# Kernel optimization log

Measured on AMD Instinct MI355X. Metric: run time of the kernel, lower is better.

## Reference

```python
import jax, jax.numpy as jnp
import numpy as np

LN_EPS = 1e-5

def _conv2d(x, w, b, pad):
    # x: [B,C,H,W], w: [O,I,kh,kw] -> [B,O,H,W]
    y = jax.lax.conv_general_dilated(
        x, w, window_strides=(1, 1), padding=[(pad, pad), (pad, pad)],
        dimension_numbers=('NCHW', 'OIHW', 'NCHW'))
    return y + b[None, :, None, None]

def setup_inputs() -> dict:
    key = jax.random.key(0)
    ks = jax.random.split(key, 12)
    B, C, H, W = 4, 256, 64, 64
    D = 64  # inner_projection
    s_in = 1.0 / np.sqrt(C)
    s_d1 = 1.0 / np.sqrt(D)
    s_d3 = 1.0 / np.sqrt(D * 9)
    return {
        'x':     jax.random.normal(ks[0], (B, C, H, W), jnp.float32),
        'w_in':  jax.random.normal(ks[1], (D, C, 1, 1), jnp.float32) * s_in,
        'b_in':  jnp.zeros((D,), jnp.float32),
        'wq':    jax.random.normal(ks[2], (D, D, 3, 3), jnp.float32) * s_d3,
        'bq':    jnp.zeros((D,), jnp.float32),
        'wk':    jax.random.normal(ks[3], (D, D, 3, 3), jnp.float32) * s_d3,
        'bk':    jnp.zeros((D,), jnp.float32),
        'wv':    jax.random.normal(ks[4], (D, D, 3, 3), jnp.float32) * s_d3,
        'bv':    jnp.zeros((D,), jnp.float32),
        'w_out': jax.random.normal(ks[5], (C, D, 1, 1), jnp.float32) * s_d1,
        'b_out': jnp.zeros((C,), jnp.float32),
        'gamma': jax.random.normal(ks[6], (1,), jnp.float32) * 0.1,
        'ln_w':  jnp.ones((C,), jnp.float32),
        'ln_b':  jnp.zeros((C,), jnp.float32),
    }

def _attention(q, k, v):
    # full-pixel attention, NO 1/sqrt(d) scale (matches source)
    B, C, H, W = v.shape
    N = H * W
    qf = q.reshape(B, -1, N)   # [B,d,N]
    kf = k.reshape(B, -1, N)
    vf = v.reshape(B, -1, N)
    energy = jnp.einsum('bci,bcj->bij', qf, kf)      # [B,N,N] = Q^T K
    attn = jax.nn.softmax(energy, axis=-1)
    out = jnp.einsum('bcj,bij->bci', vf, attn)        # V @ attn^T
    return out.reshape(B, C, H, W)

def _layernorm2d(x, w, b):
    # normalize over channel dim per pixel (LayerNorm2d)
    mu = jnp.mean(x, axis=1, keepdims=True)
    var = jnp.var(x, axis=1, keepdims=True)
    xn = (x - mu) * jax.lax.rsqrt(var + LN_EPS)
    return xn * w[None, :, None, None] + b[None, :, None, None]

def reference(x, w_in, b_in, wq, bq, wk, bk, wv, bv, w_out, b_out, gamma, ln_w, ln_b):
    att = _conv2d(x, w_in, b_in, 0)          # inner projection [B,D,H,W]
    q = _conv2d(att, wq, bq, 1)
    k = _conv2d(att, wk, bk, 1)
    v = _conv2d(att, wv, bv, 1)
    att = _attention(q, k, v)
    att = _conv2d(att, w_out, b_out, 0)       # outer projection [B,C,H,W]
    return _layernorm2d(gamma * x + att, ln_w, ln_b)
```

## Files before the change

kernel.cpp:

```cpp
#include <hip/hip_runtime.h>
#include <hip/hip_bf16.h>

#define BB 4
#define CC 256
#define DD 64
#define HH 64
#define WW 64
#define NN 4096
#define NSPLIT 4

typedef __hip_bfloat16 bf16;
typedef __attribute__((ext_vector_type(8))) short bf16x8;
typedef __attribute__((ext_vector_type(4))) float f32x4;
typedef __attribute__((ext_vector_type(4))) short s16x4;

#define MFMA16(a, b, c) __builtin_amdgcn_mfma_f32_16x16x32_bf16(a, b, c, 0, 0, 0)

static __device__ __forceinline__ float ldin(const void* p, size_t i, bool isb) {
  return isb ? __bfloat162float(((const bf16*)p)[i]) : ((const float*)p)[i];
}
static __device__ __forceinline__ void stout(void* p, size_t i, float v, bool isb) {
  if (isb) ((bf16*)p)[i] = __float2bfloat16(v);
  else     ((float*)p)[i] = v;
}
static __device__ __forceinline__ unsigned pack2(bf16 a, bf16 b) {
  unsigned short ua = *reinterpret_cast<unsigned short*>(&a);
  unsigned short ub = *reinterpret_cast<unsigned short*>(&b);
  return (unsigned)ua | ((unsigned)ub << 16);
}

__global__ void k_flag(const unsigned* __restrict__ lnw, int* __restrict__ flag) {
  if (threadIdx.x == 0) flag[0] = (lnw[0] == 0x3F803F80u) ? 1 : 0;
}

__global__ __launch_bounds__(256) void k_wt(
    const void* __restrict__ wq, const void* __restrict__ wk,
    const void* __restrict__ wv, const void* __restrict__ w_in,
    const void* __restrict__ w_out,
    bf16* __restrict__ Wth, bf16* __restrict__ Wtl,
    bf16* __restrict__ Win_h, bf16* __restrict__ Win_l,
    bf16* __restrict__ Wo_h, bf16* __restrict__ Wo_l,
    const int* __restrict__ flag) {
  const bool isb = flag[0] != 0;
  int u = blockIdx.x * 256 + threadIdx.x;
  if (u < 110592) {
    int c3 = u / 36864, rem = u % 36864;
    int tap = rem / 4096, r2 = rem % 4096;
    int oc = r2 >> 6, ic = r2 & 63;
    const void* w = (c3 == 0) ? wq : ((c3 == 1) ? wk : wv);
    float v = ldin(w, (size_t)oc * 576 + ic * 9 + tap, isb);
    bf16 h = __float2bfloat16(v);
    Wth[u] = h;
    Wtl[u] = __float2bfloat16(v - __bfloat162float(h));
  } else if (u < 126976) {
    int v2 = u - 110592;
    float v = ldin(w_in, v2, isb);
    bf16 h = __float2bfloat16(v);
    Win_h[v2] = h;
    Win_l[v2] = __float2bfloat16(v - __bfloat162float(h));
  } else {
    int v2 = u - 126976;
    float v = ldin(w_out, v2, isb);
    bf16 h = __float2bfloat16(v);
    Wo_h[v2] = h;
    Wo_l[v2] = __float2bfloat16(v - __bfloat162float(h));
  }
}

__global__ __launch_bounds__(256) void k_conv_in(
    const void* __restrict__ x,
    const bf16* __restrict__ Win_h, const bf16* __restrict__ Win_l,
    const void* __restrict__ bias, bf16* __restrict__ att_h,
    bf16* __restrict__ att_l, const int* __restrict__ flag) {
  __shared__ __align__(16) short Xh[64 * 64];
  __shared__ __align__(16) short Xl[64 * 64];
  const bool isb = flag[0] != 0;
  const int b = blockIdx.y, n0 = blockIdx.x * 64;
  const int t = threadIdx.x;
  const int w = t >> 6, lane = t & 63, quad = lane >> 4, l16 = lane & 15;
  const int l7 = l16 & 7;
  const size_t xoff = (size_t)b * CC * NN;
  f32x4 acc[4];
  #pragma unroll
  for (int nt = 0; nt < 4; ++nt)
    #pragma unroll
    for (int r = 0; r < 4; ++r)
      acc[nt][r] = ldin(bias, w * 16 + quad * 4 + r, isb);
  for (int c0 = 0; c0 < CC; c0 += 64) {
    __syncthreads();
    #pragma unroll
    for (int i = 0; i < 8; ++i) {
      int u = t + i * 256;
      int dd = u >> 6, n = u & 63;
      float v0 = ldin(x, xoff + (size_t)(c0 + 2 * dd) * NN + n0 + n, isb);
      float v1 = ldin(x, xoff + (size_t)(c0 + 2 * dd + 1) * NN + n0 + n, isb);
      bf16 h0 = __float2bfloat16(v0), h1 = __float2bfloat16(v1);
      bf16 l0 = __float2bfloat16(v0 - __bfloat162float(h0));
      bf16 l1 = __float2bfloat16(v1 - __bfloat162float(h1));
      int cs = ((dd >> 2) ^ (n & 7)) * 8 + ((2 * dd) & 7);
      *(unsigned*)&Xh[n * 64 + cs] = pack2(h0, h1);
      *(unsigned*)&Xl[n * 64 + cs] = pack2(l0, l1);
    }
    __syncthreads();
    #pragma unroll
    for (int kc = 0; kc < 2; ++kc) {
      size_t woff = (size_t)(w * 16 + l16) * 256 + c0 + kc * 32 + quad * 8;
      bf16x8 wh = *(const bf16x8*)(Win_h + woff);
      bf16x8 wl = *(const bf16x8*)(Win_l + woff);
      const int xo = ((kc * 4 + quad) ^ l7) * 8;
      #pragma unroll
      for (int nt = 0; nt < 4; ++nt) {
        int rn = nt * 16 + l16;
        bf16x8 xh = *(const bf16x8*)&Xh[rn * 64 + xo];
        bf16x8 xl = *(const bf16x8*)&Xl[rn * 64 + xo];
        acc[nt] = MFMA16(wh, xh, acc[nt]);
        acc[nt] = MFMA16(wh, xl, acc[nt]);
        acc[nt] = MFMA16(wl, xh, acc[nt]);
      }
    }
  }
  #pragma unroll
  for (int nt = 0; nt < 4; ++nt) {
    size_t off = ((size_t)b * NN + n0 + nt * 16 + l16) * DD + w * 16 + quad * 4;
    bf16 h[4], l[4];
    #pragma unroll
    for (int r = 0; r < 4; ++r) {
      float v = acc[nt][r];
      h[r] = __float2bfloat16(v);
      l[r] = __float2bfloat16(v - __bfloat162float(h[r]));
    }
    uint2 hv = make_uint2(pack2(h[0], h[1]), pack2(h[2], h[3]));
    uint2 lv = make_uint2(pack2(l[0], l[1]), pack2(l[2], l[3]));
    *(uint2*)&att_h[off] = hv;
    *(uint2*)&att_l[off] = lv;
  }
}

__global__ __launch_bounds__(256) void k_conv3(
    const bf16* __restrict__ att_h, const bf16* __restrict__ att_l,
    const bf16* __restrict__ Wth, const bf16* __restrict__ Wtl,
    const void* __restrict__ bq, const void* __restrict__ bk,
    const void* __restrict__ bv,
    bf16* __restrict__ qth, bf16* __restrict__ qtl,
    bf16* __restrict__ kth, bf16* __restrict__ ktl,
    bf16* __restrict__ vt, const int* __restrict__ flag) {
  __shared__ __align__(16) short Ah[3 * 66 * 72];
  __shared__ __align__(16) short Al[3 * 66 * 72];
  __shared__ float o_s[64 * 65];
  const bool isb = flag[0] != 0;
  const int y = blockIdx.x, b = blockIdx.y, c3 = blockIdx.z;
  const int t = threadIdx.x;
  const int w = t >> 6, lane = t & 63, quad = lane >> 4, l16 = lane & 15;
  const uint4 z4 = make_uint4(0, 0, 0, 0);
  #pragma unroll
  for (int r = 0; r < 3; ++r) {
    int yp = y + r - 1;
    bool ok = (unsigned)yp < 64u;
    const uint4* sh = (const uint4*)(att_h + ((size_t)b * NN + (size_t)yp * 64) * DD);
    const uint4* sl = (const uint4*)(att_l + ((size_t)b * NN + (size_t)yp * 64) * DD);
    #pragma unroll
    for (int ii = 0; ii < 2; ++ii) {
      int u = t + ii * 256;
      int xx = u >> 3, icg = (u & 7) * 8;
      uint4 vh = ok ? sh[u] : z4;
      uint4 vl = ok ? sl[u] : z4;
      *(uint4*)&Ah[r * 4752 + (xx + 1) * 72 + icg] = vh;
      *(uint4*)&Al[r * 4752 + (xx + 1) * 72 + icg] = vl;
    }
    if (t < 16) {
      int col = (t & 1) ? 65 : 0, icg = (t >> 1) * 8;
      *(uint4*)&Ah[r * 4752 + col * 72 + icg] = z4;
      *(uint4*)&Al[r * 4752 + col * 72 + icg] = z4;
    }
  }
  __syncthreads();
  const void* bp = (c3 == 0) ? bq : ((c3 == 1) ? bk : bv);
  const bf16* wth = Wth + (size_t)c3 * 9 * 4096;
  const bf16* wtl = Wtl + (size_t)c3 * 9 * 4096;
  f32x4 acc[4];
  #pragma unroll
  for (int nt = 0; nt < 4; ++nt)
    #pragma unroll
    for (int r = 0; r < 4; ++r)
      acc[nt][r] = ldin(bp, w * 16 + quad * 4 + r, isb);
  #pragma unroll
  for (int tap = 0; tap < 9; ++tap) {
    const int dy = tap / 3, dx = tap % 3;
    const int woff = tap * 4096 + (w * 16 + l16) * 64 + quad * 8;
    bf16x8 wh0 = *(const bf16x8*)(wth + woff);
    bf16x8 wh1 = *(const bf16x8*)(wth + woff + 32);
    bf16x8 wl0 = *(const bf16x8*)(wtl + woff);
    bf16x8 wl1 = *(const bf16x8*)(wtl + woff + 32);
    const int abase = dy * 4752 + (l16 + dx) * 72 + quad * 8;
    #pragma unroll
    for (int nt = 0; nt < 4; ++nt) {
      int ao2 = abase + nt * 16 * 72;
      bf16x8 ah0 = *(const bf16x8*)&Ah[ao2];
      bf16x8 ah1 = *(const bf16x8*)&Ah[ao2 + 32];
      bf16x8 al0 = *(const bf16x8*)&Al[ao2];
      bf16x8 al1 = *(const bf16x8*)&Al[ao2 + 32];
      acc[nt] = MFMA16(wh0, ah0, acc[nt]);
      acc[nt] = MFMA16(wh1, ah1, acc[nt]);
      acc[nt] = MFMA16(wh0, al0, acc[nt]);
      acc[nt] = MFMA16(wh1, al1, acc[nt]);
      acc[nt] = MFMA16(wl0, ah0, acc[nt]);
      acc[nt] = MFMA16(wl1, ah1, acc[nt]);
    }
  }
  if (c3 < 2) {
    bf16* dh = (c3 == 0) ? qth : kth;
    bf16* dl = (c3 == 0) ? qtl : ktl;
    const size_t rowb = (size_t)b * NN + (size_t)y * 64;
    #pragma unroll
    for (int nt = 0; nt < 4; ++nt) {
      size_t off = (rowb + nt * 16 + l16) * DD + w * 16 + quad * 4;
      bf16 h[4], l[4];
      #pragma unroll
      for (int r = 0; r < 4; ++r) {
        float v = acc[nt][r];
        h[r] = __float2bfloat16(v);
        l[r] = __float2bfloat16(v - __bfloat162float(h[r]));
      }
      *(uint2*)&dh[off] = make_uint2(pack2(h[0], h[1]), pack2(h[2], h[3]));
      *(uint2*)&dl[off] = make_uint2(pack2(l[0], l[1]), pack2(l[2], l[3]));
    }
  } else {
    #pragma unroll
    for (int nt = 0; nt < 4; ++nt)
      #pragma unroll
      for (int r = 0; r < 4; ++r)
        o_s[(nt * 16 + l16) * 65 + w * 16 + quad * 4 + r] = acc[nt][r];
    __syncthreads();
    #pragma unroll
    for (int i = 0; i < 8; ++i) {
      int u = t + i * 256;
      int c = u >> 5, np = (u & 31) * 2;
      float v0 = o_s[np * 65 + c], v1 = o_s[(np + 1) * 65 + c];
      *(unsigned*)&vt[((size_t)b * DD + c) * NN + (size_t)y * 64 + np] =
          pack2(__float2bfloat16(v0), __float2bfloat16(v1));
    }
  }
}

__global__ __launch_bounds__(256) void k_attn(
    const bf16* __restrict__ qth, const bf16* __restrict__ qtl,
    const bf16* __restrict__ kth, const bf16* __restrict__ ktl,
    const bf16* __restrict__ vt, float* __restrict__ po,
    float* __restrict__ pm, float* __restrict__ pl) {
  __shared__ __align__(16) short Kh[64 * 64];
  __shared__ __align__(16) short Kl[64 * 64];
  __shared__ __align__(16) short Vs[64 * 64];
  __shared__ __align__(16) short Ps[64 * 64];
  const int b = blockIdx.y, i0 = blockIdx.x * 64, sp = blockIdx.z;
  const int jt0 = sp * (64 / NSPLIT), jt1 = jt0 + (64 / NSPLIT);
  const int t = threadIdx.x;
  const int w = t >> 6, lane = t & 63, quad = lane >> 4, l16 = lane & 15;
  const int l7 = l16 & 7;
  const int xA = (quad ^ l7) * 8;
  const int xB = ((quad + 4) ^ l7) * 8;
  const int sr = t >> 2, m4 = t & 3, sg = m4 * 16;
  const int sc0 = ((2 * m4) ^ (sr & 7)) * 8;
  const int sc1 = ((2 * m4 + 1) ^ (sr & 7)) * 8;
  {
    size_t off = ((size_t)b * NN + i0 + sr) * DD + sg;
    const uint4* qh = (const uint4*)(qth + off);
    const uint4* ql = (const uint4*)(qtl + off);
    *(uint4*)&Kh[sr * 64 + sc0] = qh[0];
    *(uint4*)&Kh[sr * 64 + sc1] = qh[1];
    *(uint4*)&Kl[sr * 64 + sc0] = ql[0];
    *(uint4*)&Kl[sr * 64 + sc1] = ql[1];
  }
  uint4 kh0, kh1, kl0, kl1, vx0, vx1;
  {
    size_t koff = ((size_t)b * NN + jt0 * 64 + sr) * DD + sg;
    kh0 = ((const uint4*)(kth + koff))[0]; kh1 = ((const uint4*)(kth + koff))[1];
    kl0 = ((const uint4*)(ktl + koff))[0]; kl1 = ((const uint4*)(ktl + koff))[1];
    size_t voff = ((size_t)b * DD + sr) * NN + jt0 * 64 + sg;
    vx0 = ((const uint4*)(vt + voff))[0];  vx1 = ((const uint4*)(vt + voff))[1];
  }
  __syncthreads();
  const int rq = w * 16 + l16;
  const bf16x8 qf_h0 = *(const bf16x8*)&Kh[rq * 64 + xA];
  const bf16x8 qf_h1 = *(const bf16x8*)&Kh[rq * 64 + xB];
  const bf16x8 qf_l0 = *(const bf16x8*)&Kl[rq * 64 + xA];
  const bf16x8 qf_l1 = *(const bf16x8*)&Kl[rq * 64 + xB];
  float m_run = -1e30f, l_run = 0.f;
  f32x4 oacc[4] = {};
  for (int jt = jt0; jt < jt1; ++jt) {
    __syncthreads();
    *(uint4*)&Kh[sr * 64 + sc0] = kh0;    *(uint4*)&Kh[sr * 64 + sc1] = kh1;
    *(uint4*)&Kl[sr * 64 + sc0] = kl0;    *(uint4*)&Kl[sr * 64 + sc1] = kl1;
    *(uint4*)&Vs[sr * 64 + sc0] = vx0;    *(uint4*)&Vs[sr * 64 + sc1] = vx1;
    __syncthreads();
    if (jt < jt1 - 1) {
      int j0n = (jt + 1) * 64;
      size_t koff = ((size_t)b * NN + j0n + sr) * DD + sg;
      kh0 = ((const uint4*)(kth + koff))[0]; kh1 = ((const uint4*)(kth + koff))[1];
      kl0 = ((const uint4*)(ktl + koff))[0]; kl1 = ((const uint4*)(ktl + koff))[1];
      size_t voff = ((size_t)b * DD + sr) * NN + j0n + sg;
      vx0 = ((const uint4*)(vt + voff))[0];  vx1 = ((const uint4*)(vt + voff))[1];
    }
    f32x4 s[4];
    #pragma unroll
    for (int mt = 0; mt < 4; ++mt) {
      int r0 = (mt * 16 + l16) * 64;
      bf16x8 kf_h0 = *(const bf16x8*)&Kh[r0 + xA];
      bf16x8 kf_h1 = *(const bf16x8*)&Kh[r0 + xB];
      bf16x8 kf_l0 = *(const bf16x8*)&Kl[r0 + xA];
      bf16x8 kf_l1 = *(const bf16x8*)&Kl[r0 + xB];
      f32x4 c = {0.f, 0.f, 0.f, 0.f};
      c = MFMA16(kf_h0, qf_h0, c);
      c = MFMA16(kf_h1, qf_h1, c);
      c = MFMA16(kf_h0, qf_l0, c);
      c = MFMA16(kf_h1, qf_l1, c);
      c = MFMA16(kf_l0, qf_h0, c);
      c = MFMA16(kf_l1, qf_h1, c);
      s[mt] = c;
    }
    float pmax = -1e30f;
    #pragma unroll
    for (int mt = 0; mt < 4; ++mt)
      #pragma unroll
      for (int r = 0; r < 4; ++r) pmax = fmaxf(pmax, s[mt][r]);
    pmax = fmaxf(pmax, __shfl_xor(pmax, 16, 64));
    pmax = fmaxf(pmax, __shfl_xor(pmax, 32, 64));
    float m_new = fmaxf(m_run, pmax);
    float alpha = __expf(m_run - m_new);
    m_run = m_new;
    float psum = 0.f;
    short pb[16];
    #pragma unroll
    for (int mt = 0; mt < 4; ++mt)
      #pragma unroll
      for (int r = 0; r < 4; ++r) {
        float p = __expf(s[mt][r] - m_new);
        bf16 ph = __float2bfloat16(p);
        psum += __bfloat162float(ph);
        pb[mt * 4 + r] = *reinterpret_cast<short*>(&ph);
      }
    psum += __shfl_xor(psum, 16, 64);
    psum += __shfl_xor(psum, 32, 64);
    l_run = l_run * alpha + psum;
    #pragma unroll
    for (int mt = 0; mt < 4; ++mt) {
      s16x4 pk;
      pk.x = pb[mt * 4 + 0]; pk.y = pb[mt * 4 + 1];
      pk.z = pb[mt * 4 + 2]; pk.w = pb[mt * 4 + 3];
      int chP = ((2 * mt + (quad >> 1)) ^ l7) * 8 + (quad & 1) * 4;
      *(s16x4*)&Ps[rq * 64 + chP] = pk;
      #pragma unroll
      for (int r = 0; r < 4; ++r) oacc[mt][r] *= alpha;
    }
    bf16x8 pf0 = *(const bf16x8*)&Ps[rq * 64 + xA];
    bf16x8 pf1 = *(const bf16x8*)&Ps[rq * 64 + xB];
    #pragma unroll
    for (int mt = 0; mt < 4; ++mt) {
      int r0 = (mt * 16 + l16) * 64;
      bf16x8 vf0 = *(const bf16x8*)&Vs[r0 + xA];
      bf16x8 vf1 = *(const bf16x8*)&Vs[r0 + xB];
      oacc[mt] = MFMA16(vf0, pf0, oacc[mt]);
      oacc[mt] = MFMA16(vf1, pf1, oacc[mt]);
    }
  }
  const int ig = i0 + w * 16 + l16;
  const size_t SEGC = (size_t)BB * DD * NN;
  #pragma unroll
  for (int mt = 0; mt < 4; ++mt)
    #pragma unroll
    for (int r = 0; r < 4; ++r) {
      int c = mt * 16 + quad * 4 + r;
      po[(size_t)sp * SEGC + ((size_t)b * DD + c) * NN + ig] = oacc[mt][r];
    }
  if (quad == 0) {
    pm[((size_t)sp * BB + b) * NN + ig] = m_run;
    pl[((size_t)sp * BB + b) * NN + ig] = l_run;
  }
}

__global__ __launch_bounds__(256) void k_amerge(
    float* __restrict__ po, const float* __restrict__ pm,
    const float* __restrict__ pl) {
  const int b = blockIdx.y, n0 = blockIdx.x * 64;
  const int t = threadIdx.x;
  const int i = n0 + (t & 63), cg = t >> 6;
  const size_t SEGC = (size_t)BB * DD * NN;
  float m[NSPLIT], ws[NSPLIT];
  float mmax = -1e30f;
  #pragma unroll
  for (int s = 0; s < NSPLIT; ++s) {
    m[s] = pm[((size_t)s * BB + b) * NN + i];
    mmax = fmaxf(mmax, m[s]);
  }
  float lsum = 0.f;
  #pragma unroll
  for (int s = 0; s < NSPLIT; ++s) {
    ws[s] = __expf(m[s] - mmax);
    lsum += ws[s] * pl[((size_t)s * BB + b) * NN + i];
  }
  float inv = 1.f / lsum;
  #pragma unroll
  for (int k = 0; k < 16; ++k) {
    int c = cg + k * 4;
    size_t slot = ((size_t)b * DD + c) * NN + i;
    float acc = 0.f;
    #pragma unroll
    for (int s = 0; s < NSPLIT; ++s)
      acc += ws[s] * po[(size_t)s * SEGC + slot];
    po[slot] = acc * inv;
  }
}

__global__ __launch_bounds__(256) void k_out_ln(
    const float* __restrict__ ao, const void* __restrict__ x,
    const bf16* __restrict__ Wo_h, const bf16* __restrict__ Wo_l,
    const void* __restrict__ bias, const void* __restrict__ gamma,
    const void* __restrict__ lw, const void* __restrict__ lb,
    void* __restrict__ out, const int* __restrict__ flag) {
  __shared__ __align__(16) short Ahs[64 * 64];
  __shared__ __align__(16) short Als[64 * 64];
  __shared__ float red1[64 * 4], red2[64 * 4];
  __shared__ float mu_s[64], rs_s[64];
  __shared__ float lw_s[256], lb_s[256];
  const bool isb = flag[0] != 0;
  const int b = blockIdx.y, n0 = blockIdx.x * 64;
  const int t = threadIdx.x;
  const int w = t >> 6, lane = t & 63, quad = lane >> 4, l16 = lane & 15;
  const int l7 = l16 & 7;
  #pragma unroll
  for (int i = 0; i < 8; ++i) {
    int u = t + i * 256;
    int dd = u >> 6, n = u & 63;
    float v0 = ao[((size_t)b * DD + 2 * dd) * NN + n0 + n];
    float v1 = ao[((size_t)b * DD + 2 * dd + 1) * NN + n0 + n];
    bf16 h0 = __float2bfloat16(v0), h1 = __float2bfloat16(v1);
    bf16 l0 = __float2bfloat16(v0 - __bfloat162float(h0));
    bf16 l1 = __float2bfloat16(v1 - __bfloat162float(h1));
    int cs = ((dd >> 2) ^ (n & 7)) * 8 + ((2 * dd) & 7);
    *(unsigned*)&Ahs[n * 64 + cs] = pack2(h0, h1);
    *(unsigned*)&Als[n * 64 + cs] = pack2(l0, l1);
  }
  lw_s[t] = ldin(lw, t, isb);
  lb_s[t] = ldin(lb, t, isb);
  const float g = ldin(gamma, 0, isb);
  f32x4 acc[4][4];
  #pragma unroll
  for (int oct = 0; oct < 4; ++oct)
    #pragma unroll
    for (int r = 0; r < 4; ++r) {
      float bo = ldin(bias, w * 64 + oct * 16 + quad * 4 + r, isb);
      #pragma unroll
      for (int nt = 0; nt < 4; ++nt) acc[oct][nt][r] = bo;
    }
  __syncthreads();
  #pragma unroll
  for (int oct = 0; oct < 4; ++oct) {
    const int base = w * 64 + oct * 16;
    #pragma unroll
    for (int kc = 0; kc < 2; ++kc) {
      size_t woff = (size_t)(base + l16) * 64 + kc * 32 + quad * 8;
      bf16x8 wh = *(const bf16x8*)(Wo_h + woff);
      bf16x8 wl = *(const bf16x8*)(Wo_l + woff);
      const int xo = ((kc * 4 + quad) ^ l7) * 8;
      #pragma unroll
      for (int nt = 0; nt < 4; ++nt) {
        int rn = nt * 16 + l16;
        bf16x8 ah = *(const bf16x8*)&Ahs[rn * 64 + xo];
        bf16x8 al = *(const bf16x8*)&Als[rn * 64 + xo];
        acc[oct][nt] = MFMA16(wh, ah, acc[oct][nt]);
        acc[oct][nt] = MFMA16(wh, al, acc[oct][nt]);
        acc[oct][nt] = MFMA16(wl, ah, acc[oct][nt]);
      }
    }
  }
  #pragma unroll
  for (int nt = 0; nt < 4; ++nt) {
    int nn = nt * 16 + l16;
    float s1 = 0.f, s2 = 0.f;
    #pragma unroll
    for (int oct = 0; oct < 4; ++oct)
      #pragma unroll
      for (int r = 0; r < 4; ++r) {
        int oc = w * 64 + oct * 16 + quad * 4 + r;
        float xv = ldin(x, ((size_t)b * CC + oc) * NN + n0 + nn, isb);
        float y = acc[oct][nt][r] + g * xv;
        acc[oct][nt][r] = y;
        s1 += y; s2 += y * y;
      }
    s1 += __shfl_xor(s1, 16, 64); s1 += __shfl_xor(s1, 32, 64);
    s2 += __shfl_xor(s2, 16, 64); s2 += __shfl_xor(s2, 32, 64);
    if (quad == 0) { red1[nn * 4 + w] = s1; red2[nn * 4 + w] = s2; }
  }
  __syncthreads();
  if (t < 64) {
    float sm = red1[t * 4] + red1[t * 4 + 1] + red1[t * 4 + 2] + red1[t * 4 + 3];
    float sq = red2[t * 4] + red2[t * 4 + 1] + red2[t * 4 + 2] + red2[t * 4 + 3];
    float mu = sm * (1.f / 256.f);
    float var = sq * (1.f / 256.f) - mu * mu;
    mu_s[t] = mu;
    rs_s[t] = rsqrtf(var + 1e-5f);
  }
  __syncthreads();
  #pragma unroll
  for (int nt = 0; nt < 4; ++nt) {
    int nn = nt * 16 + l16;
    float mu = mu_s[nn], rs = rs_s[nn];
    #pragma unroll
    for (int oct = 0; oct < 4; ++oct)
      #pragma unroll
      for (int r = 0; r < 4; ++r) {
        int oc = w * 64 + oct * 16 + quad * 4 + r;
        float o = (acc[oct][nt][r] - mu) * rs * lw_s[oc] + lb_s[oc];
        stout(out, ((size_t)b * CC + oc) * NN + n0 + nn, o, isb);
      }
  }
}

extern "C" void kernel_launch(void* const* d_in, const int* in_sizes, int n_in,
                              void* d_out, int out_size, void* d_ws, size_t ws_size,
                              hipStream_t stream) {
  const void* x     = d_in[0];
  const void* w_in  = d_in[1];
  const void* b_in  = d_in[2];
  const void* wq    = d_in[3];
  const void* bq    = d_in[4];
  const void* wk    = d_in[5];
  const void* bk    = d_in[6];
  const void* wv    = d_in[7];
  const void* bv    = d_in[8];
  const void* w_out = d_in[9];
  const void* b_out = d_in[10];
  const void* gamma = d_in[11];
  const void* ln_w  = d_in[12];
  const void* ln_b  = d_in[13];

  const size_t SEG = (size_t)BB * DD * NN;
  int*   flag  = (int*)d_ws;
  char*  p     = (char*)d_ws + 64;
  bf16*  att_h = (bf16*)p;  p += SEG * 2;
  bf16*  att_l = (bf16*)p;  p += SEG * 2;
  bf16*  qth   = (bf16*)p;  p += SEG * 2;
  bf16*  qtl   = (bf16*)p;  p += SEG * 2;
  bf16*  kth   = (bf16*)p;  p += SEG * 2;
  bf16*  ktl   = (bf16*)p;  p += SEG * 2;
  bf16*  vt    = (bf16*)p;  p += SEG * 2;
  float* po    = (float*)p; p += (size_t)NSPLIT * SEG * 4;
  float* pm    = (float*)p; p += (size_t)NSPLIT * BB * NN * 4;
  float* pl    = (float*)p; p += (size_t)NSPLIT * BB * NN * 4;
  bf16*  Wth   = (bf16*)p;  p += 110592 * 2;
  bf16*  Wtl   = (bf16*)p;  p += 110592 * 2;
  bf16*  Win_h = (bf16*)p;  p += 16384 * 2;
  bf16*  Win_l = (bf16*)p;  p += 16384 * 2;
  bf16*  Wo_h  = (bf16*)p;  p += 16384 * 2;
  bf16*  Wo_l  = (bf16*)p;  p += 16384 * 2;

  k_flag<<<1, 64, 0, stream>>>((const unsigned*)ln_w, flag);
  k_wt<<<560, 256, 0, stream>>>(wq, wk, wv, w_in, w_out, Wth, Wtl,
                                Win_h, Win_l, Wo_h, Wo_l, flag);
  k_conv_in<<<dim3(NN / 64, BB), 256, 0, stream>>>(x, Win_h, Win_l, b_in,
                                                   att_h, att_l, flag);
  k_conv3<<<dim3(64, BB, 3), 256, 0, stream>>>(att_h, att_l, Wth, Wtl,
                                               bq, bk, bv,
                                               qth, qtl, kth, ktl, vt, flag);
  k_attn<<<dim3(NN / 64, BB, NSPLIT), 256, 0, stream>>>(qth, qtl, kth, ktl, vt,
                                                        po, pm, pl);
  k_amerge<<<dim3(NN / 64, BB), 256, 0, stream>>>(po, pm, pl);
  k_out_ln<<<dim3(NN / 64, BB), 256, 0, stream>>>(po, x, Wo_h, Wo_l, b_out,
                                                  gamma, ln_w, ln_b, d_out, flag);
}
```

Before: 204.6 us.

## Fuse split-attention merge into output projection, double split count, halve pixel tiles

Removes the separate k_amerge kernel and folds the split-softmax merge into k_out_ln: each block computes normalized per-split weights in shared memory and combines the partial outputs while staging the projection input. NSPLIT rises from 4 to 8 so the attention kernel launches more blocks. k_conv_in and k_out_ln now use 32-pixel tiles, doubling their grid sizes. This drops one launch and one round trip of the merged result through global memory, but doubles the partial-output buffer that must be written and read, and the smaller tiles give less weight reuse per block.

```diff
diff --git a/kernel.cpp b/kernel.cpp
--- a/kernel.cpp
+++ b/kernel.cpp
@@ -7,7 +7,7 @@
 #define HH 64
 #define WW 64
 #define NN 4096
-#define NSPLIT 4
+#define NSPLIT 8
 
 typedef __hip_bfloat16 bf16;
 typedef __attribute__((ext_vector_type(8))) short bf16x8;
@@ -72,26 +72,26 @@
     const bf16* __restrict__ Win_h, const bf16* __restrict__ Win_l,
     const void* __restrict__ bias, bf16* __restrict__ att_h,
     bf16* __restrict__ att_l, const int* __restrict__ flag) {
-  __shared__ __align__(16) short Xh[64 * 64];
-  __shared__ __align__(16) short Xl[64 * 64];
+  __shared__ __align__(16) short Xh[32 * 64];
+  __shared__ __align__(16) short Xl[32 * 64];
   const bool isb = flag[0] != 0;
-  const int b = blockIdx.y, n0 = blockIdx.x * 64;
+  const int b = blockIdx.y, n0 = blockIdx.x * 32;
   const int t = threadIdx.x;
   const int w = t >> 6, lane = t & 63, quad = lane >> 4, l16 = lane & 15;
   const int l7 = l16 & 7;
   const size_t xoff = (size_t)b * CC * NN;
-  f32x4 acc[4];
-  #pragma unroll
-  for (int nt = 0; nt < 4; ++nt)
+  f32x4 acc[2];
+  #pragma unroll
+  for (int nt = 0; nt < 2; ++nt)
     #pragma unroll
     for (int r = 0; r < 4; ++r)
       acc[nt][r] = ldin(bias, w * 16 + quad * 4 + r, isb);
   for (int c0 = 0; c0 < CC; c0 += 64) {
     __syncthreads();
     #pragma unroll
-    for (int i = 0; i < 8; ++i) {
+    for (int i = 0; i < 4; ++i) {
       int u = t + i * 256;
-      int dd = u >> 6, n = u & 63;
+      int dd = u >> 5, n = u & 31;
       float v0 = ldin(x, xoff + (size_t)(c0 + 2 * dd) * NN + n0 + n, isb);
       float v1 = ldin(x, xoff + (size_t)(c0 + 2 * dd + 1) * NN + n0 + n, isb);
       bf16 h0 = __float2bfloat16(v0), h1 = __float2bfloat16(v1);
@@ -109,7 +109,7 @@
       bf16x8 wl = *(const bf16x8*)(Win_l + woff);
       const int xo = ((kc * 4 + quad) ^ l7) * 8;
       #pragma unroll
-      for (int nt = 0; nt < 4; ++nt) {
+      for (int nt = 0; nt < 2; ++nt) {
         int rn = nt * 16 + l16;
         bf16x8 xh = *(const bf16x8*)&Xh[rn * 64 + xo];
         bf16x8 xl = *(const bf16x8*)&Xl[rn * 64 + xo];
@@ -120,7 +120,7 @@
     }
   }
   #pragma unroll
-  for (int nt = 0; nt < 4; ++nt) {
+  for (int nt = 0; nt < 2; ++nt) {
     size_t off = ((size_t)b * NN + n0 + nt * 16 + l16) * DD + w * 16 + quad * 4;
     bf16 h[4], l[4];
     #pragma unroll
@@ -129,10 +129,8 @@
       h[r] = __float2bfloat16(v);
       l[r] = __float2bfloat16(v - __bfloat162float(h[r]));
     }
-    uint2 hv = make_uint2(pack2(h[0], h[1]), pack2(h[2], h[3]));
-    uint2 lv = make_uint2(pack2(l[0], l[1]), pack2(l[2], l[3]));
-    *(uint2*)&att_h[off] = hv;
-    *(uint2*)&att_l[off] = lv;
+    *(uint2*)&att_h[off] = make_uint2(pack2(h[0], h[1]), pack2(h[2], h[3]));
+    *(uint2*)&att_l[off] = make_uint2(pack2(l[0], l[1]), pack2(l[2], l[3]));
   }
 }
 
@@ -377,61 +375,60 @@
   }
 }
 
-__global__ __launch_bounds__(256) void k_amerge(
-    float* __restrict__ po, const float* __restrict__ pm,
-    const float* __restrict__ pl) {
-  const int b = blockIdx.y, n0 = blockIdx.x * 64;
-  const int t = threadIdx.x;
-  const int i = n0 + (t & 63), cg = t >> 6;
-  const size_t SEGC = (size_t)BB * DD * NN;
-  float m[NSPLIT], ws[NSPLIT];
-  float mmax = -1e30f;
-  #pragma unroll
-  for (int s = 0; s < NSPLIT; ++s) {
-    m[s] = pm[((size_t)s * BB + b) * NN + i];
-    mmax = fmaxf(mmax, m[s]);
-  }
-  float lsum = 0.f;
-  #pragma unroll
-  for (int s = 0; s < NSPLIT; ++s) {
-    ws[s] = __expf(m[s] - mmax);
-    lsum += ws[s] * pl[((size_t)s * BB + b) * NN + i];
-  }
-  float inv = 1.f / lsum;
-  #pragma unroll
-  for (int k = 0; k < 16; ++k) {
-    int c = cg + k * 4;
-    size_t slot = ((size_t)b * DD + c) * NN + i;
-    float acc = 0.f;
-    #pragma unroll
-    for (int s = 0; s < NSPLIT; ++s)
-      acc += ws[s] * po[(size_t)s * SEGC + slot];
-    po[slot] = acc * inv;
-  }
-}
-
 __global__ __launch_bounds__(256) void k_out_ln(
-    const float* __restrict__ ao, const void* __restrict__ x,
+    const float* __restrict__ po, const float* __restrict__ pm,
+    const float* __restrict__ pl, const void* __restrict__ x,
     const bf16* __restrict__ Wo_h, const bf16* __restrict__ Wo_l,
     const void* __restrict__ bias, const void* __restrict__ gamma,
     const void* __restrict__ lw, const void* __restrict__ lb,
     void* __restrict__ out, const int* __restrict__ flag) {
-  __shared__ __align__(16) short Ahs[64 * 64];
-  __shared__ __align__(16) short Als[64 * 64];
-  __shared__ float red1[64 * 4], red2[64 * 4];
-  __shared__ float mu_s[64], rs_s[64];
+  __shared__ __align__(16) short Ahs[32 * 64];
+  __shared__ __align__(16) short Als[32 * 64];
+  __shared__ float wsn[NSPLIT][32];
+  __shared__ float red1[32 * 4], red2[32 * 4];
+  __shared__ float mu_s[32], rs_s[32];
   __shared__ float lw_s[256], lb_s[256];
   const bool isb = flag[0] != 0;
-  const int b = blockIdx.y, n0 = blockIdx.x * 64;
+  const int b = blockIdx.y, n0 = blockIdx.x * 32;
   const int t = threadIdx.x;
   const int w = t >> 6, lane = t & 63, quad = lane >> 4, l16 = lane & 15;
   const int l7 = l16 & 7;
-  #pragma unroll
-  for (int i = 0; i < 8; ++i) {
+  const size_t SEGC = (size_t)BB * DD * NN;
+  if (t < 32) {
+    int i = n0 + t;
+    float m[NSPLIT], ws[NSPLIT];
+    float mmax = -1e30f;
+    #pragma unroll
+    for (int s = 0; s < NSPLIT; ++s) {
+      m[s] = pm[((size_t)s * BB + b) * NN + i];
+      mmax = fmaxf(mmax, m[s]);
+    }
+    float lsum = 0.f;
+    #pragma unroll
+    for (int s = 0; s < NSPLIT; ++s) {
+      ws[s] = __expf(m[s] - mmax);
+      lsum += ws[s] * pl[((size_t)s * BB + b) * NN + i];
+    }
+    float inv = 1.f / lsum;
+    #pragma unroll
+    for (int s = 0; s < NSPLIT; ++s) wsn[s][t] = ws[s] * inv;
+  }
+  lw_s[t] = ldin(lw, t, isb);
+  lb_s[t] = ldin(lb, t, isb);
+  const float g = ldin(gamma, 0, isb);
+  __syncthreads();
+  #pragma unroll
+  for (int i = 0; i < 4; ++i) {
     int u = t + i * 256;
-    int dd = u >> 6, n = u & 63;
-    float v0 = ao[((size_t)b * DD + 2 * dd) * NN + n0 + n];
-    float v1 = ao[((size_t)b * DD + 2 * dd + 1) * NN + n0 + n];
+    int dd = u >> 5, n = u & 31;
+    size_t base = ((size_t)b * DD + 2 * dd) * NN + n0 + n;
+    float v0 = 0.f, v1 = 0.f;
+    #pragma unroll
+    for (int s = 0; s < NSPLIT; ++s) {
+      float wv = wsn[s][n];
+      v0 += wv * po[(size_t)s * SEGC + base];
+      v1 += wv * po[(size_t)s * SEGC + base + NN];
+    }
     bf16 h0 = __float2bfloat16(v0), h1 = __float2bfloat16(v1);
     bf16 l0 = __float2bfloat16(v0 - __bfloat162float(h0));
     bf16 l1 = __float2bfloat16(v1 - __bfloat162float(h1));
@@ -439,17 +436,14 @@
     *(unsigned*)&Ahs[n * 64 + cs] = pack2(h0, h1);
     *(unsigned*)&Als[n * 64 + cs] = pack2(l0, l1);
   }
-  lw_s[t] = ldin(lw, t, isb);
-  lb_s[t] = ldin(lb, t, isb);
-  const float g = ldin(gamma, 0, isb);
-  f32x4 acc[4][4];
+  f32x4 acc[4][2];
   #pragma unroll
   for (int oct = 0; oct < 4; ++oct)
     #pragma unroll
     for (int r = 0; r < 4; ++r) {
       float bo = ldin(bias, w * 64 + oct * 16 + quad * 4 + r, isb);
       #pragma unroll
-      for (int nt = 0; nt < 4; ++nt) acc[oct][nt][r] = bo;
+      for (int nt = 0; nt < 2; ++nt) acc[oct][nt][r] = bo;
     }
   __syncthreads();
   #pragma unroll
@@ -462,7 +456,7 @@
       bf16x8 wl = *(const bf16x8*)(Wo_l + woff);
       const int xo = ((kc * 4 + quad) ^ l7) * 8;
       #pragma unroll
-      for (int nt = 0; nt < 4; ++nt) {
+      for (int nt = 0; nt < 2; ++nt) {
         int rn = nt * 16 + l16;
         bf16x8 ah = *(const bf16x8*)&Ahs[rn * 64 + xo];
         bf16x8 al = *(const bf16x8*)&Als[rn * 64 + xo];
@@ -473,7 +467,7 @@
     }
   }
   #pragma unroll
-  for (int nt = 0; nt < 4; ++nt) {
+  for (int nt = 0; nt < 2; ++nt) {
     int nn = nt * 16 + l16;
     float s1 = 0.f, s2 = 0.f;
     #pragma unroll
@@ -491,7 +485,7 @@
     if (quad == 0) { red1[nn * 4 + w] = s1; red2[nn * 4 + w] = s2; }
   }
   __syncthreads();
-  if (t < 64) {
+  if (t < 32) {
     float sm = red1[t * 4] + red1[t * 4 + 1] + red1[t * 4 + 2] + red1[t * 4 + 3];
     float sq = red2[t * 4] + red2[t * 4 + 1] + red2[t * 4 + 2] + red2[t * 4 + 3];
     float mu = sm * (1.f / 256.f);
@@ -501,7 +495,7 @@
   }
   __syncthreads();
   #pragma unroll
-  for (int nt = 0; nt < 4; ++nt) {
+  for (int nt = 0; nt < 2; ++nt) {
     int nn = nt * 16 + l16;
     float mu = mu_s[nn], rs = rs_s[nn];
     #pragma unroll
@@ -556,14 +550,14 @@
   k_flag<<<1, 64, 0, stream>>>((const unsigned*)ln_w, flag);
   k_wt<<<560, 256, 0, stream>>>(wq, wk, wv, w_in, w_out, Wth, Wtl,
                                 Win_h, Win_l, Wo_h, Wo_l, flag);
-  k_conv_in<<<dim3(NN / 64, BB), 256, 0, stream>>>(x, Win_h, Win_l, b_in,
+  k_conv_in<<<dim3(NN / 32, BB), 256, 0, stream>>>(x, Win_h, Win_l, b_in,
                                                    att_h, att_l, flag);
   k_conv3<<<dim3(64, BB, 3), 256, 0, stream>>>(att_h, att_l, Wth, Wtl,
                                                bq, bk, bv,
                                                qth, qtl, kth, ktl, vt, flag);
   k_attn<<<dim3(NN / 64, BB, NSPLIT), 256, 0, stream>>>(qth, qtl, kth, ktl, vt,
                                                         po, pm, pl);
-  k_amerge<<<dim3(NN / 64, BB), 256, 0, stream>>>(po, pm, pl);
-  k_out_ln<<<dim3(NN / 64, BB), 256, 0, stream>>>(po, x, Wo_h, Wo_l, b_out,
-                                                  gamma, ln_w, ln_b, d_out, flag);
-}
+  k_out_ln<<<dim3(NN / 32, BB), 256, 0, stream>>>(po, pm, pl, x, Wo_h, Wo_l,
+                                                  b_out, gamma, ln_w, ln_b,
+                                                  d_out, flag);
+}
```

After: 198.9 us. -2.8%, faster.
